# Performance work log

Measured on AMD Instinct MI355X. Metric: run time of the kernel, lower is better.

## Reference

```python
import jax, jax.numpy as jnp
import numpy as np

B, L, C_IN, D, H, DFF, NL, NC, PH = 32, 512, 16, 512, 8, 2048, 3, 10, 128
DH = D // H


def circ_conv1d(x, w):
    # x: [B, C, S] with circular padding 1 on spatial dim, w: [O, C, 3]
    xp = jnp.concatenate([x[..., -1:], x, x[..., :1]], axis=-1)
    return jax.lax.conv_general_dilated(xp, w, (1,), 'VALID',
                                        dimension_numbers=('NCH', 'OIH', 'NCH'))


def positional_embedding(length, d):
    pos = jnp.arange(length, dtype=jnp.float32)[:, None]
    div = jnp.exp(jnp.arange(0, d, 2, dtype=jnp.float32) * (-np.log(10000.0) / d))
    pe = jnp.zeros((length, d), jnp.float32)
    pe = pe.at[:, 0::2].set(jnp.sin(pos * div))
    pe = pe.at[:, 1::2].set(jnp.cos(pos * div))
    return pe


def layer_norm(x, g, b):
    m = jnp.mean(x, -1, keepdims=True)
    v = jnp.var(x, -1, keepdims=True)
    return (x - m) / jnp.sqrt(v + 1e-5) * g + b


def projector(x, stats, conv_w, w0, b0, w1, b1, w2):
    # x: [B, L, C_IN] (channels = seq_len, spatial = enc_in), stats: [B, 1, C_IN]
    y = circ_conv1d(x, conv_w)                     # [B, 1, C_IN]
    y = jnp.concatenate([y, stats], axis=1)        # [B, 2, C_IN]
    y = y.reshape(x.shape[0], -1)                  # [B, 2*C_IN]
    h = jax.nn.relu(y @ w0.T + b0)
    h = jax.nn.relu(h @ w1.T + b1)
    return h @ w2.T                                # no bias on output


def setup_inputs() -> dict:
    key = jax.random.key(0)
    ks = iter(jax.random.split(key, 64))
    rn = lambda shape, s=0.02: jax.random.normal(next(ks), shape, jnp.float32) * s
    inp = {
        'x_enc': jax.random.normal(next(ks), (B, L, C_IN), jnp.float32),
        'x_mark_enc': jnp.ones((B, L), jnp.float32),
        'tok_w': rn((D, C_IN, 3)),
        'Wq': rn((NL, D, D)), 'bq': jnp.zeros((NL, D)),
        'Wk': rn((NL, D, D)), 'bk': jnp.zeros((NL, D)),
        'Wv': rn((NL, D, D)), 'bv': jnp.zeros((NL, D)),
        'Wo': rn((NL, D, D)), 'bo': jnp.zeros((NL, D)),
        'W1': rn((NL, DFF, D)), 'b1': jnp.zeros((NL, DFF)),
        'W2': rn((NL, D, DFF)), 'b2': jnp.zeros((NL, D)),
        'ln1_g': jnp.ones((NL, D)), 'ln1_b': jnp.zeros((NL, D)),
        'ln2_g': jnp.ones((NL, D)), 'ln2_b': jnp.zeros((NL, D)),
        'norm_g': jnp.ones((D,)), 'norm_b': jnp.zeros((D,)),
        'proj_w': rn((NC, D * L)), 'proj_b': jnp.zeros((NC,)),
        'tau_conv_w': rn((1, L, 3)), 'tau_w0': rn((PH, 2 * C_IN)), 'tau_b0': jnp.zeros((PH,)),
        'tau_w1': rn((PH, PH)), 'tau_b1': jnp.zeros((PH,)), 'tau_w2': rn((1, PH)),
        'del_conv_w': rn((1, L, 3)), 'del_w0': rn((PH, 2 * C_IN)), 'del_b0': jnp.zeros((PH,)),
        'del_w1': rn((PH, PH)), 'del_b1': jnp.zeros((PH,)), 'del_w2': rn((L, PH)),
    }
    return inp


def reference(x_enc, x_mark_enc, tok_w,
              Wq, bq, Wk, bk, Wv, bv, Wo, bo,
              W1, b1, W2, b2, ln1_g, ln1_b, ln2_g, ln2_b,
              norm_g, norm_b, proj_w, proj_b,
              tau_conv_w, tau_w0, tau_b0, tau_w1, tau_b1, tau_w2,
              del_conv_w, del_w0, del_b0, del_w1, del_b1, del_w2):
    # De-stationary statistics (detached in the original)
    x_raw = jax.lax.stop_gradient(x_enc)
    mean_enc = jnp.mean(x_raw, 1, keepdims=True)                 # [B,1,C]
    std_enc = jnp.sqrt(jnp.var(x_raw, 1, keepdims=True) + 1e-5)  # [B,1,C]
    tau = jnp.exp(projector(x_raw, std_enc, tau_conv_w, tau_w0, tau_b0,
                            tau_w1, tau_b1, tau_w2))             # [B,1]
    delta = projector(x_raw, mean_enc, del_conv_w, del_w0, del_b0,
                      del_w1, del_b1, del_w2)                    # [B,L]

    # DataEmbedding: circular token conv + sinusoidal positional encoding
    tok = circ_conv1d(jnp.transpose(x_enc, (0, 2, 1)), tok_w)    # [B,D,L]
    x = jnp.transpose(tok, (0, 2, 1)) + positional_embedding(L, D)[None]

    scale = 1.0 / np.sqrt(DH)
    tau4 = tau.reshape(B, 1, 1, 1)
    delta4 = delta[:, None, None, :]
    for i in range(NL):
        q = (x @ Wq[i].T + bq[i]).reshape(B, L, H, DH)
        k = (x @ Wk[i].T + bk[i]).reshape(B, L, H, DH)
        v = (x @ Wv[i].T + bv[i]).reshape(B, L, H, DH)
        scores = jnp.einsum('blhe,bshe->bhls', q, k) * tau4 + delta4
        A = jax.nn.softmax(scale * scores, axis=-1)
        o = jnp.einsum('bhls,bshd->blhd', A, v).reshape(B, L, D)
        o = o @ Wo[i].T + bo[i]
        x = layer_norm(x + o, ln1_g[i], ln1_b[i])
        y = jax.nn.gelu(x @ W1[i].T + b1[i], approximate=False) @ W2[i].T + b2[i]
        x = layer_norm(x + y, ln2_g[i], ln2_b[i])
    x = layer_norm(x, norm_g, norm_b)

    out = jax.nn.gelu(x, approximate=False)
    out = out * x_mark_enc[..., None]
    out = out.reshape(B, -1) @ proj_w.T + proj_b                 # [B, NC]
    return out
```

## Files before the change

### kernel.cpp

```cpp
#include <hip/hip_runtime.h>
#include <hip/hip_bf16.h>
#include <cstdint>

#define DEVINL __device__ __forceinline__

typedef unsigned short u16;
typedef short bf16x8 __attribute__((ext_vector_type(8)));
typedef float f32x4 __attribute__((ext_vector_type(4)));
typedef float f32x16 __attribute__((ext_vector_type(16)));

DEVINL u16 f2b(float f) {
    union { float f; uint32_t u; } x{f};
    uint32_t r = x.u + 0x7fffu + ((x.u >> 16) & 1u);
    return (u16)(r >> 16);
}
DEVINL float b2f(u16 h) {
    union { uint32_t u; float f; } x{(uint32_t)h << 16};
    return x.f;
}
DEVINL float gelu_exact(float v) {
    return 0.5f * v * (1.0f + erff(v * 0.70710678118654752f));
}
DEVINL void gload_lds16(const void* g, void* l) {
    __builtin_amdgcn_global_load_lds(
        (const __attribute__((address_space(1))) void*)(uintptr_t)g,
        (__attribute__((address_space(3))) void*)(uint32_t)(uintptr_t)l,
        16, 0, 0);
}
DEVINL void cvt8(const float* src, u16* dst) {
    float4 a = *(const float4*)src;
    float4 b = *(const float4*)(src + 4);
    u16 t[8] = {f2b(a.x), f2b(a.y), f2b(a.z), f2b(a.w),
                f2b(b.x), f2b(b.y), f2b(b.z), f2b(b.w)};
    *(uint4*)dst = *(const uint4*)t;
}

__global__ __launch_bounds__(256)
void cvtqkv_kernel(const float* __restrict__ Wq, const float* __restrict__ Wk,
                   const float* __restrict__ Wv, u16* __restrict__ dst) {
    size_t i = ((size_t)blockIdx.x * 256 + threadIdx.x) * 8;
    int slice = (int)(i >> 18);
    int layer = slice / 3, which = slice - layer * 3;
    size_t rem = i & 262143;
    const float* src = (which == 0 ? Wq : which == 1 ? Wk : Wv) + (size_t)layer * 262144 + rem;
    u16* d = dst + (size_t)layer * 786432 + (size_t)which * 262144 + rem;
    cvt8(src, d);
}
__global__ __launch_bounds__(256)
void cvt4_kernel(const float* __restrict__ s0, const float* __restrict__ s1,
                 const float* __restrict__ s2, const float* __restrict__ s3,
                 u16* __restrict__ d0, u16* __restrict__ d1,
                 u16* __restrict__ d2, u16* __restrict__ d3) {
    size_t i = ((size_t)blockIdx.x * 256 + threadIdx.x) * 8;
    if (i < 786432) { cvt8(s0 + i, d0 + i); return; }
    i -= 786432;
    if (i < 3145728) { cvt8(s1 + i, d1 + i); return; }
    i -= 3145728;
    if (i < 3145728) { cvt8(s2 + i, d2 + i); return; }
    i -= 3145728;
    if (i < 2621440) { cvt8(s3 + i, d3 + i); }
}

__global__ void packb_kernel(const float* __restrict__ bq, const float* __restrict__ bk,
                             const float* __restrict__ bv, float* __restrict__ out) {
    int idx = blockIdx.x * 256 + threadIdx.x;
    if (idx >= 3 * 1536) return;
    int i = idx / 1536, j = idx - i * 1536;
    float v = (j < 512) ? bq[i * 512 + j]
            : (j < 1024) ? bk[i * 512 + j - 512]
                         : bv[i * 512 + j - 1024];
    out[idx] = v;
}

__global__ void pe_kernel(float* __restrict__ pet) {
    int l = blockIdx.x, d2 = threadIdx.x;
    float freq = expf(-(float)(2 * d2) * 0.0179889460390f);
    float ang = (float)l * freq;
    pet[l * 512 + 2 * d2]     = sinf(ang);
    pet[l * 512 + 2 * d2 + 1] = cosf(ang);
}

__global__ void stats_kernel(const float* __restrict__ xe, float* __restrict__ mean,
                             float* __restrict__ stdv) {
    int b = blockIdx.x, ln = threadIdx.x;
    int c = ln & 15, part = ln >> 4;
    float s = 0.f, sq = 0.f;
    for (int l = part; l < 512; l += 4) {
        float x = xe[(size_t)b * 8192 + l * 16 + c];
        s += x; sq += x * x;
    }
    s += __shfl_xor(s, 16);  s += __shfl_xor(s, 32);
    sq += __shfl_xor(sq, 16); sq += __shfl_xor(sq, 32);
    if (part == 0) {
        float m = s * (1.0f / 512.0f);
        mean[b * 16 + c] = m;
        stdv[b * 16 + c] = sqrtf(sq * (1.0f / 512.0f) - m * m + 1e-5f);
    }
}

__global__ __launch_bounds__(128)
void proj_kernel(const float* __restrict__ xe, const float* __restrict__ stats,
                 const float* __restrict__ cw, const float* __restrict__ w0,
                 const float* __restrict__ b0, const float* __restrict__ w1,
                 const float* __restrict__ b1, const float* __restrict__ w2,
                 float* __restrict__ outp, int outn, int do_exp) {
    __shared__ float zl[32], h0l[128], h1l[128], red[2];
    int b = blockIdx.x, tid = threadIdx.x;
    {
        int c = tid >> 3, part = tid & 7;
        float acc = 0.f;
        for (int l = part; l < 512; l += 8) {
            const float* xr = xe + (size_t)b * 8192 + l * 16;
            float w0v = cw[l * 3 + 0], w1v = cw[l * 3 + 1], w2v = cw[l * 3 + 2];
            acc += xr[(c + 15) & 15] * w0v + xr[c] * w1v + xr[(c + 1) & 15] * w2v;
        }
        acc += __shfl_xor(acc, 1); acc += __shfl_xor(acc, 2); acc += __shfl_xor(acc, 4);
        if (part == 0) zl[c] = acc;
        if (tid < 16) zl[16 + tid] = stats[b * 16 + tid];
    }
    __syncthreads();
    {
        float acc = b0[tid];
        #pragma unroll
        for (int i = 0; i < 32; ++i) acc += zl[i] * w0[tid * 32 + i];
        h0l[tid] = fmaxf(acc, 0.0f);
    }
    __syncthreads();
    {
        float acc = b1[tid];
        for (int i = 0; i < 128; ++i) acc += h0l[i] * w1[tid * 128 + i];
        h1l[tid] = fmaxf(acc, 0.0f);
    }
    __syncthreads();
    if (outn == 1) {
        float p = h1l[tid] * w2[tid];
        p += __shfl_xor(p, 1);  p += __shfl_xor(p, 2);  p += __shfl_xor(p, 4);
        p += __shfl_xor(p, 8);  p += __shfl_xor(p, 16); p += __shfl_xor(p, 32);
        if ((tid & 63) == 0) red[tid >> 6] = p;
        __syncthreads();
        if (tid == 0) {
            float v = red[0] + red[1];
            outp[b] = do_exp ? expf(v) : v;
        }
    } else {
        for (int l = tid; l < outn; l += 128) {
            float acc = 0.f;
            for (int i = 0; i < 128; ++i) acc += h1l[i] * w2[l * 128 + i];
            outp[(size_t)b * outn + l] = acc;
        }
    }
}

__global__ __launch_bounds__(256)
void tokconv_kernel(const float* __restrict__ xe, const float* __restrict__ tw,
                    const float* __restrict__ pet,
                    float* __restrict__ xf, u16* __restrict__ xb) {
    __shared__ float xs[34][16];
    int lt = blockIdx.x, b = blockIdx.y, tid = threadIdx.x;
    int l0 = lt * 32;
    for (int idx = tid; idx < 34 * 16; idx += 256) {
        int r = idx >> 4, c = idx & 15;
        int gl = (l0 - 1 + r + 512) & 511;
        xs[r][c] = xe[(size_t)b * 8192 + gl * 16 + c];
    }
    __syncthreads();
    for (int dd = tid; dd < 512; dd += 256) {
        float twr[48];
        #pragma unroll
        for (int i = 0; i < 48; ++i) twr[i] = tw[dd * 48 + i];
        for (int l = 0; l < 32; ++l) {
            float acc = 0.f;
            #pragma unroll
            for (int c = 0; c < 16; ++c) {
                acc += xs[l][c]     * twr[c * 3 + 0];
                acc += xs[l + 1][c] * twr[c * 3 + 1];
                acc += xs[l + 2][c] * twr[c * 3 + 2];
            }
            float vv = acc + pet[(size_t)(l0 + l) * 512 + dd];
            size_t idx = ((size_t)b * 512 + l0 + l) * 512 + dd;
            xf[idx] = vv;
            xb[idx] = f2b(vv);
        }
    }
}

template <int ACT>
__global__ __launch_bounds__(256)
void gemm32(const u16* __restrict__ A, const u16* __restrict__ B,
            const float* __restrict__ bias, u16* __restrict__ Cv0,
            u16* __restrict__ Cv1, int M, int N, int K, int Kc) {
    __shared__ u16 smem[3][2][128 * 32];
    const int tid = threadIdx.x, wv = tid >> 6, ln = tid & 63;
    const int nwg = gridDim.x * gridDim.y;
    const int bid = blockIdx.y * gridDim.x + blockIdx.x;
    const int wg  = (bid & 7) * (nwg >> 3) + (bid >> 3);
    const int n0 = (wg % gridDim.x) * 128;
    const int m0 = (wg / gridDim.x) * 128;
    const int kz = blockIdx.z;
    const int wm = (wv >> 1) * 64, wn = (wv & 1) * 64;
    const int l31 = ln & 31, h2 = ln >> 5;
    f32x16 acc[2][2] = {};
    const int r0s = wv * 16 + (ln >> 2);
    const int sl = ln & 3;
    const int k0 = kz * Kc;

    auto stage = [&](int buf, int kt) {
        #pragma unroll
        for (int c = 0; c < 2; ++c) {
            int row = r0s + c * 64;
            int ssl = sl ^ ((row >> 1) & 3);
            int ldsoff = row * 32 + sl * 8;
            gload_lds16(A + (size_t)(m0 + row) * K + kt + ssl * 8, (char*)smem[buf][0] + ldsoff * 2);
            gload_lds16(B + (size_t)(n0 + row) * K + kt + ssl * 8, (char*)smem[buf][1] + ldsoff * 2);
        }
    };

    const int nt = Kc >> 5;
    stage(0, k0);
    if (nt > 1) stage(1, k0 + 32);
    for (int t = 0; t < nt; ++t) {
        if (t + 1 < nt) { asm volatile("s_waitcnt vmcnt(4)"); }
        else            { asm volatile("s_waitcnt vmcnt(0)"); }
        __builtin_amdgcn_s_barrier();
        if (t + 2 < nt) stage((t + 2) % 3, k0 + (t + 2) * 32);
        const u16* As = smem[t % 3][0];
        const u16* Bs = smem[t % 3][1];
        bf16x8 af[2][2], bfr[2][2];
        #pragma unroll
        for (int mi = 0; mi < 2; ++mi) {
            int row = wm + mi * 32 + l31;
            int swz = (row >> 1) & 3;
            #pragma unroll
            for (int kk = 0; kk < 2; ++kk) {
                int phys = (kk * 2 + h2) ^ swz;
                af[mi][kk] = *(const bf16x8*)(As + row * 32 + phys * 8);
            }
        }
        #pragma unroll
        for (int nj = 0; nj < 2; ++nj) {
            int row = wn + nj * 32 + l31;
            int swz = (row >> 1) & 3;
            #pragma unroll
            for (int kk = 0; kk < 2; ++kk) {
                int phys = (kk * 2 + h2) ^ swz;
                bfr[nj][kk] = *(const bf16x8*)(Bs + row * 32 + phys * 8);
            }
        }
        #pragma unroll
        for (int mi = 0; mi < 2; ++mi)
            #pragma unroll
            for (int nj = 0; nj < 2; ++nj)
                #pragma unroll
                for (int kk = 0; kk < 2; ++kk)
                    acc[mi][nj] = __builtin_amdgcn_mfma_f32_32x32x16_bf16(
                        af[mi][kk], bfr[nj][kk], acc[mi][nj], 0, 0, 0);
    }
    __syncthreads();

    const bool second = (kz != 0);
    float* eps = (float*)smem + wv * (16 * 68);
    u16* Cout = second ? Cv1 : Cv0;
    #pragma unroll
    for (int ch = 0; ch < 4; ++ch) {
        const int mi = ch >> 1, rsel = ch & 1;
        #pragma unroll
        for (int nj = 0; nj < 2; ++nj) {
            int col = nj * 32 + l31;
            float bv = second ? 0.0f : bias[n0 + wn + col];
            #pragma unroll
            for (int r1l = 0; r1l < 2; ++r1l)
                #pragma unroll
                for (int rr = 0; rr < 4; ++rr) {
                    int reg = rr + 4 * (rsel * 2 + r1l);
                    int rloc = h2 * 4 + rr + 8 * r1l;
                    float v = acc[mi][nj][reg] + bv;
                    if (ACT == 1 && !second) v = gelu_exact(v);
                    eps[rloc * 68 + col] = v;
                }
        }
        #pragma unroll
        for (int pp = 0; pp < 4; ++pp) {
            int rl = pp * 4 + (ln >> 4);
            float4 vv = *(const float4*)(eps + rl * 68 + (ln & 15) * 4);
            size_t row = (size_t)(m0 + wm + ch * 16 + rl);
            int col = n0 + wn + (ln & 15) * 4;
            u16 t4[4] = {f2b(vv.x), f2b(vv.y), f2b(vv.z), f2b(vv.w)};
            *(uint2*)(Cout + row * N + col) = *(const uint2*)t4;
        }
    }
}

__global__ __launch_bounds__(512)
void attn2_kernel(const u16* __restrict__ qkv, const float* __restrict__ tau,
                  const float* __restrict__ delta, u16* __restrict__ o) {
    __shared__ u16 KL[64 * 64];
    __shared__ u16 VT[64 * 72];
    __shared__ u16 PL[8][32 * 64];
    const int tid = threadIdx.x, w = tid >> 6, ln = tid & 63;
    const int lo = ln & 15, hi = ln >> 4;
    const int qh = blockIdx.x, h = blockIdx.y, b = blockIdx.z;
    const size_t qrow0 = (size_t)b * 512;
    const u16* qp = qkv;
    const u16* kp = qkv + 512;
    const u16* vp = qkv + 1024;
    const int hofs = h * 64;
    const float ts = tau[b] * 0.125f;
    u16* Pw = (u16*)PL[w];
    const int q0 = qh * 256 + w * 32;

    bf16x8 qa[2][2];
    #pragma unroll
    for (int i = 0; i < 2; ++i)
        #pragma unroll
        for (int ks = 0; ks < 2; ++ks)
            qa[i][ks] = *(const bf16x8*)(qp + (qrow0 + q0 + i * 16 + lo) * 1536 + hofs + ks * 32 + hi * 8);

    float m_run[2] = {-1e30f, -1e30f};
    float l_run[2] = {0.f, 0.f};
    f32x4 oacc[2][4] = {};

    const int vsl = tid & 7, vsr = tid >> 3;
    uint4 vreg = *(const uint4*)(vp + (qrow0 + vsr) * 1536 + hofs + vsl * 8);

    for (int nt = 0; nt < 8; ++nt) {
        __syncthreads();
        {
            int s = tid >> 3, j = tid & 7;
            int jl = j ^ (s & 7);
            gload_lds16(kp + (qrow0 + nt * 64 + s) * 1536 + hofs + jl * 8,
                        (char*)KL + tid * 16);
        }
        {
            u16 tmp[8]; *(uint4*)tmp = vreg;
            #pragma unroll
            for (int e = 0; e < 8; ++e) {
                int d = vsl * 8 + e;
                int byt = d * 144 + (((vsr >> 3) ^ vsl) << 4) + (vsr & 7) * 2;
                *(u16*)((char*)VT + byt) = tmp[e];
            }
        }
        if (nt < 7)
            vreg = *(const uint4*)(vp + (qrow0 + (nt + 1) * 64 + vsr) * 1536 + hofs + vsl * 8);
        __syncthreads();

        f32x4 sacc[2][4] = {};
        #pragma unroll
        for (int ks = 0; ks < 2; ++ks) {
            #pragma unroll
            for (int jn = 0; jn < 4; ++jn) {
                int s = jn * 16 + lo;
                int phys = (ks * 4 + hi) ^ (s & 7);
                bf16x8 kb = *(const bf16x8*)((const char*)KL + s * 128 + phys * 16);
                #pragma unroll
                for (int i = 0; i < 2; ++i)
                    sacc[i][jn] = __builtin_amdgcn_mfma_f32_16x16x32_bf16(kb, qa[i][ks], sacc[i][jn], 0, 0, 0);
            }
        }
        float tmax[2] = {-1e30f, -1e30f};
        #pragma unroll
        for (int jn = 0; jn < 4; ++jn) {
            float4 dv4 = *(const float4*)(delta + b * 512 + nt * 64 + jn * 16 + hi * 4);
            float dv[4] = {dv4.x, dv4.y, dv4.z, dv4.w};
            #pragma unroll
            for (int i = 0; i < 2; ++i)
                #pragma unroll
                for (int r = 0; r < 4; ++r) {
                    float v = sacc[i][jn][r] * ts + dv[r] * 0.125f;
                    sacc[i][jn][r] = v;
                    tmax[i] = fmaxf(tmax[i], v);
                }
        }
        #pragma unroll
        for (int i = 0; i < 2; ++i) {
            tmax[i] = fmaxf(tmax[i], __shfl_xor(tmax[i], 16));
            tmax[i] = fmaxf(tmax[i], __shfl_xor(tmax[i], 32));
            float mnew = fmaxf(m_run[i], tmax[i]);
            float fac = __expf(m_run[i] - mnew);
            m_run[i] = mnew;
            l_run[i] *= fac;
            #pragma unroll
            for (int jd = 0; jd < 4; ++jd)
                #pragma unroll
                for (int r = 0; r < 4; ++r) oacc[i][jd][r] *= fac;
        }
        #pragma unroll
        for (int i = 0; i < 2; ++i) {
            float ls = 0.f;
            #pragma unroll
            for (int jn = 0; jn < 4; ++jn) {
                float p0 = __expf(sacc[i][jn][0] - m_run[i]);
                float p1 = __expf(sacc[i][jn][1] - m_run[i]);
                float p2 = __expf(sacc[i][jn][2] - m_run[i]);
                float p3 = __expf(sacc[i][jn][3] - m_run[i]);
                ls += (p0 + p1) + (p2 + p3);
                uint2 pk;
                pk.x = (uint32_t)f2b(p0) | ((uint32_t)f2b(p1) << 16);
                pk.y = (uint32_t)f2b(p2) | ((uint32_t)f2b(p3) << 16);
                int q = i * 16 + lo;
                int ls16 = jn * 2 + (hi >> 1);
                int byt = q * 128 + (((ls16 ^ (q & 7)) << 4)) + (hi & 1) * 8;
                *(uint2*)((char*)Pw + byt) = pk;
            }
            ls += __shfl_xor(ls, 16);
            ls += __shfl_xor(ls, 32);
            l_run[i] += ls;
        }
        #pragma unroll
        for (int ks2 = 0; ks2 < 2; ++ks2) {
            bf16x8 pa[2];
            #pragma unroll
            for (int i = 0; i < 2; ++i) {
                int q = i * 16 + lo;
                int phys = (ks2 * 4 + hi) ^ (q & 7);
                pa[i] = *(const bf16x8*)((const char*)Pw + q * 128 + phys * 16);
            }
            #pragma unroll
            for (int jd = 0; jd < 4; ++jd) {
                int d = jd * 16 + lo;
                int cs = (ks2 * 4 + hi) ^ ((d >> 3) & 7);
                bf16x8 vb = *(const bf16x8*)((const char*)VT + d * 144 + cs * 16);
                #pragma unroll
                for (int i = 0; i < 2; ++i)
                    oacc[i][jd] = __builtin_amdgcn_mfma_f32_16x16x32_bf16(vb, pa[i], oacc[i][jd], 0, 0, 0);
            }
        }
    }
    #pragma unroll
    for (int i = 0; i < 2; ++i) {
        float inv = 1.0f / l_run[i];
        #pragma unroll
        for (int jd = 0; jd < 4; ++jd) {
            u16 t4[4];
            #pragma unroll
            for (int r = 0; r < 4; ++r) t4[r] = f2b(oacc[i][jd][r] * inv);
            size_t row = qrow0 + q0 + i * 16 + lo;
            *(uint2*)(o + row * 512 + hofs + jd * 16 + hi * 4) = *(const uint2*)t4;
        }
    }
}

__global__ __launch_bounds__(256)
void ln3_kernel(const float* __restrict__ xin, const u16* res0,
                const u16* res1, const float* __restrict__ g,
                const float* __restrict__ bta,
                float* __restrict__ xout, u16* xbf) {
    const int row = blockIdx.x * 4 + (threadIdx.x >> 6);
    const int ln = threadIdx.x & 63;
    const float* xr = xin + (size_t)row * 512;
    const u16* r0p = res0 + (size_t)row * 512;
    const u16* r1p = res1 + (size_t)row * 512;
    float4 a = *(const float4*)(xr + ln * 4);
    float4 c = *(const float4*)(xr + 256 + ln * 4);
    uint2 qa_ = *(const uint2*)(r0p + ln * 4);
    uint2 qc_ = *(const uint2*)(r0p + 256 + ln * 4);
    uint2 pa_ = *(const uint2*)(r1p + ln * 4);
    uint2 pc_ = *(const uint2*)(r1p + 256 + ln * 4);
    const u16* qa16 = (const u16*)&qa_;  const u16* qc16 = (const u16*)&qc_;
    const u16* pa16 = (const u16*)&pa_;  const u16* pc16 = (const u16*)&pc_;
    a.x += b2f(qa16[0]) + b2f(pa16[0]); a.y += b2f(qa16[1]) + b2f(pa16[1]);
    a.z += b2f(qa16[2]) + b2f(pa16[2]); a.w += b2f(qa16[3]) + b2f(pa16[3]);
    c.x += b2f(qc16[0]) + b2f(pc16[0]); c.y += b2f(qc16[1]) + b2f(pc16[1]);
    c.z += b2f(qc16[2]) + b2f(pc16[2]); c.w += b2f(qc16[3]) + b2f(pc16[3]);
    float s = a.x + a.y + a.z + a.w + c.x + c.y + c.z + c.w;
    float sq = a.x*a.x + a.y*a.y + a.z*a.z + a.w*a.w + c.x*c.x + c.y*c.y + c.z*c.z + c.w*c.w;
    #pragma unroll
    for (int m = 1; m < 64; m <<= 1) { s += __shfl_xor(s, m); sq += __shfl_xor(sq, m); }
    float mean = s * 0.001953125f;
    float var = sq * 0.001953125f - mean * mean;
    float rstd = rsqrtf(var + 1e-5f);
    float4 g0 = *(const float4*)(g + ln * 4);
    float4 g1 = *(const float4*)(g + 256 + ln * 4);
    float4 b0 = *(const float4*)(bta + ln * 4);
    float4 b1 = *(const float4*)(bta + 256 + ln * 4);
    float4 o0, o1;
    o0.x = (a.x - mean) * rstd * g0.x + b0.x;
    o0.y = (a.y - mean) * rstd * g0.y + b0.y;
    o0.z = (a.z - mean) * rstd * g0.z + b0.z;
    o0.w = (a.w - mean) * rstd * g0.w + b0.w;
    o1.x = (c.x - mean) * rstd * g1.x + b1.x;
    o1.y = (c.y - mean) * rstd * g1.y + b1.y;
    o1.z = (c.z - mean) * rstd * g1.z + b1.z;
    o1.w = (c.w - mean) * rstd * g1.w + b1.w;
    *(float4*)(xout + (size_t)row * 512 + ln * 4) = o0;
    *(float4*)(xout + (size_t)row * 512 + 256 + ln * 4) = o1;
    u16 t0[4] = {f2b(o0.x), f2b(o0.y), f2b(o0.z), f2b(o0.w)};
    u16 t1[4] = {f2b(o1.x), f2b(o1.y), f2b(o1.z), f2b(o1.w)};
    *(uint2*)(xbf + (size_t)row * 512 + ln * 4) = *(const uint2*)t0;
    *(uint2*)(xbf + (size_t)row * 512 + 256 + ln * 4) = *(const uint2*)t1;
}

__global__ __launch_bounds__(256)
void lngelu_kernel(const float* __restrict__ xin, const float* __restrict__ g,
                   const float* __restrict__ bta, const float* __restrict__ mark,
                   u16* __restrict__ outb) {
    const int row = blockIdx.x * 4 + (threadIdx.x >> 6);
    const int ln = threadIdx.x & 63;
    const float* xr = xin + (size_t)row * 512;
    float4 a = *(const float4*)(xr + ln * 4);
    float4 c = *(const float4*)(xr + 256 + ln * 4);
    float s = a.x + a.y + a.z + a.w + c.x + c.y + c.z + c.w;
    float sq = a.x*a.x + a.y*a.y + a.z*a.z + a.w*a.w + c.x*c.x + c.y*c.y + c.z*c.z + c.w*c.w;
    #pragma unroll
    for (int m = 1; m < 64; m <<= 1) { s += __shfl_xor(s, m); sq += __shfl_xor(sq, m); }
    float mean = s * 0.001953125f;
    float var = sq * 0.001953125f - mean * mean;
    float rstd = rsqrtf(var + 1e-5f);
    float mk = mark[row];
    float4 g0 = *(const float4*)(g + ln * 4);
    float4 g1 = *(const float4*)(g + 256 + ln * 4);
    float4 b0 = *(const float4*)(bta + ln * 4);
    float4 b1 = *(const float4*)(bta + 256 + ln * 4);
    float v0 = gelu_exact((a.x - mean) * rstd * g0.x + b0.x) * mk;
    float v1 = gelu_exact((a.y - mean) * rstd * g0.y + b0.y) * mk;
    float v2 = gelu_exact((a.z - mean) * rstd * g0.z + b0.z) * mk;
    float v3 = gelu_exact((a.w - mean) * rstd * g0.w + b0.w) * mk;
    float v4 = gelu_exact((c.x - mean) * rstd * g1.x + b1.x) * mk;
    float v5 = gelu_exact((c.y - mean) * rstd * g1.y + b1.y) * mk;
    float v6 = gelu_exact((c.z - mean) * rstd * g1.z + b1.z) * mk;
    float v7 = gelu_exact((c.w - mean) * rstd * g1.w + b1.w) * mk;
    u16 t0[4] = {f2b(v0), f2b(v1), f2b(v2), f2b(v3)};
    u16 t1[4] = {f2b(v4), f2b(v5), f2b(v6), f2b(v7)};
    *(uint2*)(outb + (size_t)row * 512 + ln * 4) = *(const uint2*)t0;
    *(uint2*)(outb + (size_t)row * 512 + 256 + ln * 4) = *(const uint2*)t1;
}

__global__ __launch_bounds__(256)
void fproj_kernel(const u16* __restrict__ gb, const u16* __restrict__ pw,
                  const float* __restrict__ pb, float* __restrict__ out) {
    __shared__ float red[32][4];
    int n = blockIdx.x, ks = blockIdx.y, tid = threadIdx.x;
    float acc[32];
    #pragma unroll
    for (int m = 0; m < 32; ++m) acc[m] = 0.f;
    for (int j = 0; j < 8; ++j) {
        size_t k0 = (size_t)ks * 16384 + j * 2048 + tid * 8;
        bf16x8 w8 = *(const bf16x8*)(pw + (size_t)n * 262144 + k0);
        float wf[8];
        #pragma unroll
        for (int e = 0; e < 8; ++e) wf[e] = b2f((u16)w8[e]);
        #pragma unroll
        for (int m = 0; m < 32; ++m) {
            bf16x8 g8 = *(const bf16x8*)(gb + (size_t)m * 262144 + k0);
            float a = acc[m];
            #pragma unroll
            for (int e = 0; e < 8; ++e) a += b2f((u16)g8[e]) * wf[e];
            acc[m] = a;
        }
    }
    int w = tid >> 6;
    #pragma unroll
    for (int m = 0; m < 32; ++m) {
        float s = acc[m];
        s += __shfl_xor(s, 1);  s += __shfl_xor(s, 2);  s += __shfl_xor(s, 4);
        s += __shfl_xor(s, 8);  s += __shfl_xor(s, 16); s += __shfl_xor(s, 32);
        if ((tid & 63) == 0) red[m][w] = s;
    }
    __syncthreads();
    if (tid < 32) {
        int m = tid;
        float s = red[m][0] + red[m][1] + red[m][2] + red[m][3];
        if (ks == 0) s += pb[n];
        atomicAdd(&out[m * 10 + n], s);
    }
}

extern "C" void kernel_launch(void* const* d_in, const int* in_sizes, int n_in,
                              void* d_out, int out_size, void* d_ws, size_t ws_size,
                              hipStream_t stream) {
    const float* x_enc  = (const float*)d_in[0];
    const float* x_mark = (const float*)d_in[1];
    const float* tok_w  = (const float*)d_in[2];
    const float* Wq = (const float*)d_in[3];   const float* bq = (const float*)d_in[4];
    const float* Wk = (const float*)d_in[5];   const float* bk = (const float*)d_in[6];
    const float* Wv = (const float*)d_in[7];   const float* bv = (const float*)d_in[8];
    const float* Wo = (const float*)d_in[9];   const float* bo = (const float*)d_in[10];
    const float* W1 = (const float*)d_in[11];  const float* b1 = (const float*)d_in[12];
    const float* W2 = (const float*)d_in[13];  const float* b2 = (const float*)d_in[14];
    const float* ln1_g = (const float*)d_in[15]; const float* ln1_b = (const float*)d_in[16];
    const float* ln2_g = (const float*)d_in[17]; const float* ln2_b = (const float*)d_in[18];
    const float* norm_g = (const float*)d_in[19]; const float* norm_b = (const float*)d_in[20];
    const float* proj_w = (const float*)d_in[21]; const float* proj_b = (const float*)d_in[22];
    const float* tau_cw = (const float*)d_in[23];
    const float* tau_w0 = (const float*)d_in[24]; const float* tau_b0 = (const float*)d_in[25];
    const float* tau_w1 = (const float*)d_in[26]; const float* tau_b1 = (const float*)d_in[27];
    const float* tau_w2 = (const float*)d_in[28];
    const float* del_cw = (const float*)d_in[29];
    const float* del_w0 = (const float*)d_in[30]; const float* del_b0 = (const float*)d_in[31];
    const float* del_w1 = (const float*)d_in[32]; const float* del_b1 = (const float*)d_in[33];
    const float* del_w2 = (const float*)d_in[34];
    float* out = (float*)d_out;

    char* ws = (char*)d_ws;
    size_t off = 0;
    auto alloc = [&](size_t bytes) -> void* {
        void* p = ws + off;
        off += (bytes + 255) & ~(size_t)255;
        return p;
    };
    u16* wqkvb = (u16*)alloc((size_t)3 * 786432 * 2);
    u16* wob = (u16*)alloc(786432 * 2);
    u16* w1b = (u16*)alloc(3145728 * 2);
    u16* w2b = (u16*)alloc(3145728 * 2);
    u16* pwb = (u16*)alloc(2621440 * 2);
    float* bqkvb = (float*)alloc(3 * 1536 * 4);
    float* petab = (float*)alloc((size_t)262144 * 4);
    float* meanb = (float*)alloc(512 * 4);
    float* stdb  = (float*)alloc(512 * 4);
    float* taub  = (float*)alloc(32 * 4);
    float* delb  = (float*)alloc(16384 * 4);
    float* xf = (float*)alloc((size_t)8388608 * 4);
    u16*  xb  = (u16*)alloc((size_t)8388608 * 2);
    u16*  sfb = (u16*)alloc((size_t)8388608 * 2);
    u16* qkvb = (u16*)alloc((size_t)16384 * 1536 * 2);
    u16* ob   = (u16*)alloc((size_t)8388608 * 2);
    u16* hb   = qkvb;
    u16* gbuf = qkvb;
    u16* p1o  = qkvb;
    u16* p1f  = xb;

    cvtqkv_kernel<<<dim3(1152), dim3(256), 0, stream>>>(Wq, Wk, Wv, wqkvb);
    cvt4_kernel<<<dim3(5030), dim3(256), 0, stream>>>(Wo, W1, W2, proj_w, wob, w1b, w2b, pwb);
    packb_kernel<<<dim3(18), dim3(256), 0, stream>>>(bq, bk, bv, bqkvb);
    pe_kernel<<<dim3(512), dim3(256), 0, stream>>>(petab);

    stats_kernel<<<dim3(32), dim3(64), 0, stream>>>(x_enc, meanb, stdb);
    proj_kernel<<<dim3(32), dim3(128), 0, stream>>>(x_enc, stdb, tau_cw, tau_w0, tau_b0,
                                                    tau_w1, tau_b1, tau_w2, taub, 1, 1);
    proj_kernel<<<dim3(32), dim3(128), 0, stream>>>(x_enc, meanb, del_cw, del_w0, del_b0,
                                                    del_w1, del_b1, del_w2, delb, 512, 0);
    tokconv_kernel<<<dim3(16, 32), dim3(256), 0, stream>>>(x_enc, tok_w, petab, xf, xb);

    for (int i = 0; i < 3; ++i) {
        const u16* wqkv_i = wqkvb + (size_t)i * 786432;
        const u16* wo_i = wob + (size_t)i * 262144;
        const u16* w1_i = w1b + (size_t)i * 1048576;
        const u16* w2_i = w2b + (size_t)i * 1048576;
        gemm32<0><<<dim3(12, 128, 1), dim3(256), 0, stream>>>(
            xb, wqkv_i, bqkvb + i * 1536, qkvb, nullptr, 16384, 1536, 512, 512);
        attn2_kernel<<<dim3(2, 8, 32), dim3(512), 0, stream>>>(qkvb, taub, delb, ob);
        gemm32<0><<<dim3(4, 128, 2), dim3(256), 0, stream>>>(
            ob, wo_i, bo + i * 512, sfb, p1o, 16384, 512, 512, 256);
        ln3_kernel<<<dim3(4096), dim3(256), 0, stream>>>(xf, sfb, p1o,
            ln1_g + i * 512, ln1_b + i * 512, xf, xb);
        gemm32<1><<<dim3(16, 128, 1), dim3(256), 0, stream>>>(
            xb, w1_i, b1 + i * 2048, hb, nullptr, 16384, 2048, 512, 512);
        gemm32<0><<<dim3(4, 128, 2), dim3(256), 0, stream>>>(
            hb, w2_i, b2 + i * 512, sfb, p1f, 16384, 512, 2048, 1024);
        ln3_kernel<<<dim3(4096), dim3(256), 0, stream>>>(xf, sfb, p1f,
            ln2_g + i * 512, ln2_b + i * 512, xf, xb);
    }

    lngelu_kernel<<<dim3(4096), dim3(256), 0, stream>>>(xf, norm_g, norm_b, x_mark, gbuf);
    hipMemsetAsync(d_out, 0, (size_t)out_size * 4, stream);
    fproj_kernel<<<dim3(10, 16), dim3(256), 0, stream>>>(gbuf, pwb, proj_b, out);
}
```

Baseline: 980.8 us.

## Fuse output and FFN-down GEMMs with residual add and LayerNorm

Adds a gemmln kernel in which each 512-thread block computes a full 64x512 row tile and applies bias, the residual add and LayerNorm in its epilogue. It replaces both the split-K gemm32 launches and the separate ln3 kernel, removing the bf16 partial-sum buffers and their round trip. The cost is a grid of only 256 blocks. B fragments are also read straight from global memory without LDS staging, which may hurt GEMM efficiency, especially for K=2048.

```diff
diff --git a/kernel.cpp b/kernel.cpp
--- a/kernel.cpp
+++ b/kernel.cpp
@@ -188,7 +188,7 @@
 __global__ __launch_bounds__(256)
 void gemm32(const u16* __restrict__ A, const u16* __restrict__ B,
             const float* __restrict__ bias, u16* __restrict__ Cv0,
-            u16* __restrict__ Cv1, int M, int N, int K, int Kc) {
+            int M, int N, int K) {
     __shared__ u16 smem[3][2][128 * 32];
     const int tid = threadIdx.x, wv = tid >> 6, ln = tid & 63;
     const int nwg = gridDim.x * gridDim.y;
@@ -196,13 +196,11 @@
     const int wg  = (bid & 7) * (nwg >> 3) + (bid >> 3);
     const int n0 = (wg % gridDim.x) * 128;
     const int m0 = (wg / gridDim.x) * 128;
-    const int kz = blockIdx.z;
     const int wm = (wv >> 1) * 64, wn = (wv & 1) * 64;
     const int l31 = ln & 31, h2 = ln >> 5;
     f32x16 acc[2][2] = {};
     const int r0s = wv * 16 + (ln >> 2);
     const int sl = ln & 3;
-    const int k0 = kz * Kc;
 
     auto stage = [&](int buf, int kt) {
         #pragma unroll
@@ -215,14 +213,14 @@
         }
     };
 
-    const int nt = Kc >> 5;
-    stage(0, k0);
-    if (nt > 1) stage(1, k0 + 32);
+    const int nt = K >> 5;
+    stage(0, 0);
+    if (nt > 1) stage(1, 32);
     for (int t = 0; t < nt; ++t) {
         if (t + 1 < nt) { asm volatile("s_waitcnt vmcnt(4)"); }
         else            { asm volatile("s_waitcnt vmcnt(0)"); }
         __builtin_amdgcn_s_barrier();
-        if (t + 2 < nt) stage((t + 2) % 3, k0 + (t + 2) * 32);
+        if (t + 2 < nt) stage((t + 2) % 3, (t + 2) * 32);
         const u16* As = smem[t % 3][0];
         const u16* Bs = smem[t % 3][1];
         bf16x8 af[2][2], bfr[2][2];
@@ -257,16 +255,14 @@
     }
     __syncthreads();
 
-    const bool second = (kz != 0);
     float* eps = (float*)smem + wv * (16 * 68);
-    u16* Cout = second ? Cv1 : Cv0;
     #pragma unroll
     for (int ch = 0; ch < 4; ++ch) {
         const int mi = ch >> 1, rsel = ch & 1;
         #pragma unroll
         for (int nj = 0; nj < 2; ++nj) {
             int col = nj * 32 + l31;
-            float bv = second ? 0.0f : bias[n0 + wn + col];
+            float bv = bias[n0 + wn + col];
             #pragma unroll
             for (int r1l = 0; r1l < 2; ++r1l)
                 #pragma unroll
@@ -274,7 +270,7 @@
                     int reg = rr + 4 * (rsel * 2 + r1l);
                     int rloc = h2 * 4 + rr + 8 * r1l;
                     float v = acc[mi][nj][reg] + bv;
-                    if (ACT == 1 && !second) v = gelu_exact(v);
+                    if (ACT == 1) v = gelu_exact(v);
                     eps[rloc * 68 + col] = v;
                 }
         }
@@ -285,9 +281,120 @@
             size_t row = (size_t)(m0 + wm + ch * 16 + rl);
             int col = n0 + wn + (ln & 15) * 4;
             u16 t4[4] = {f2b(vv.x), f2b(vv.y), f2b(vv.z), f2b(vv.w)};
-            *(uint2*)(Cout + row * N + col) = *(const uint2*)t4;
-        }
-    }
+            *(uint2*)(Cv0 + row * N + col) = *(const uint2*)t4;
+        }
+    }
+}
+
+__global__ __launch_bounds__(512)
+void gemmln_kernel(const u16* __restrict__ A, const u16* __restrict__ B,
+                   const float* __restrict__ bias, const float* __restrict__ g,
+                   const float* __restrict__ bta,
+                   float* xf, u16* __restrict__ xb, int K) {
+    __shared__ u16 As[2][64 * 64];
+    __shared__ float redS[4][64], redQ[4][64], mst[64], rst[64];
+    const int tid = threadIdx.x, wv = tid >> 6, ln = tid & 63;
+    const int wm = wv >> 2, wn = wv & 3;
+    const int lo = ln & 15, hi = ln >> 4;
+    const int m0 = blockIdx.x * 64;
+    f32x4 acc[2][8] = {};
+
+    const int srow = tid >> 3, sj = tid & 7;
+    const int sjl = sj ^ (srow & 7);
+    auto stage = [&](int buf, int kt) {
+        gload_lds16(A + (size_t)(m0 + srow) * K + kt + sjl * 8,
+                    (char*)As[buf] + tid * 16);
+    };
+
+    const int nt = K >> 6;
+    int cur = 0;
+    stage(0, 0);
+    __syncthreads();
+    for (int t = 0; t < nt; ++t) {
+        if (t + 1 < nt) stage(cur ^ 1, (t + 1) * 64);
+        const int kt = t * 64;
+        bf16x8 bfr[8][2];
+        #pragma unroll
+        for (int j = 0; j < 8; ++j) {
+            int n = wn * 128 + j * 16 + lo;
+            #pragma unroll
+            for (int kk = 0; kk < 2; ++kk)
+                bfr[j][kk] = *(const bf16x8*)(B + (size_t)n * K + kt + kk * 32 + hi * 8);
+        }
+        bf16x8 af[2][2];
+        #pragma unroll
+        for (int i = 0; i < 2; ++i) {
+            int r = wm * 32 + i * 16 + lo;
+            #pragma unroll
+            for (int kk = 0; kk < 2; ++kk) {
+                int phys = (kk * 4 + hi) ^ (r & 7);
+                af[i][kk] = *(const bf16x8*)((const char*)As[cur] + r * 128 + phys * 16);
+            }
+        }
+        #pragma unroll
+        for (int i = 0; i < 2; ++i)
+            #pragma unroll
+            for (int j = 0; j < 8; ++j)
+                #pragma unroll
+                for (int kk = 0; kk < 2; ++kk)
+                    acc[i][j] = __builtin_amdgcn_mfma_f32_16x16x32_bf16(
+                        af[i][kk], bfr[j][kk], acc[i][j], 0, 0, 0);
+        __syncthreads();
+        cur ^= 1;
+    }
+
+    float bv[8], gl[8], bl[8];
+    #pragma unroll
+    for (int j = 0; j < 8; ++j) {
+        int col = wn * 128 + j * 16 + lo;
+        bv[j] = bias[col]; gl[j] = g[col]; bl[j] = bta[col];
+    }
+    #pragma unroll
+    for (int i = 0; i < 2; ++i)
+        #pragma unroll
+        for (int rr = 0; rr < 4; ++rr) {
+            int row = wm * 32 + i * 16 + hi * 4 + rr;
+            const float* xr = xf + (size_t)(m0 + row) * 512;
+            float ps = 0.f, pq = 0.f;
+            #pragma unroll
+            for (int j = 0; j < 8; ++j) {
+                int col = wn * 128 + j * 16 + lo;
+                float v = acc[i][j][rr] + bv[j] + xr[col];
+                acc[i][j][rr] = v;
+                ps += v; pq += v * v;
+            }
+            ps += __shfl_xor(ps, 1); pq += __shfl_xor(pq, 1);
+            ps += __shfl_xor(ps, 2); pq += __shfl_xor(pq, 2);
+            ps += __shfl_xor(ps, 4); pq += __shfl_xor(pq, 4);
+            ps += __shfl_xor(ps, 8); pq += __shfl_xor(pq, 8);
+            if (lo == 0) { redS[wn][row] = ps; redQ[wn][row] = pq; }
+        }
+    __syncthreads();
+    if (tid < 64) {
+        float s = redS[0][tid] + redS[1][tid] + redS[2][tid] + redS[3][tid];
+        float q = redQ[0][tid] + redQ[1][tid] + redQ[2][tid] + redQ[3][tid];
+        float mean = s * (1.0f / 512.0f);
+        float var = q * (1.0f / 512.0f) - mean * mean;
+        mst[tid] = mean;
+        rst[tid] = rsqrtf(var + 1e-5f);
+    }
+    __syncthreads();
+    #pragma unroll
+    for (int i = 0; i < 2; ++i)
+        #pragma unroll
+        for (int rr = 0; rr < 4; ++rr) {
+            int row = wm * 32 + i * 16 + hi * 4 + rr;
+            float mean = mst[row], rstd = rst[row];
+            float* xfo = xf + (size_t)(m0 + row) * 512;
+            u16* xbo = xb + (size_t)(m0 + row) * 512;
+            #pragma unroll
+            for (int j = 0; j < 8; ++j) {
+                int col = wn * 128 + j * 16 + lo;
+                float nv = (acc[i][j][rr] - mean) * rstd * gl[j] + bl[j];
+                xfo[col] = nv;
+                xbo[col] = f2b(nv);
+            }
+        }
 }
 
 __global__ __launch_bounds__(512)
@@ -437,56 +544,6 @@
             *(uint2*)(o + row * 512 + hofs + jd * 16 + hi * 4) = *(const uint2*)t4;
         }
     }
-}
-
-__global__ __launch_bounds__(256)
-void ln3_kernel(const float* __restrict__ xin, const u16* res0,
-                const u16* res1, const float* __restrict__ g,
-                const float* __restrict__ bta,
-                float* __restrict__ xout, u16* xbf) {
-    const int row = blockIdx.x * 4 + (threadIdx.x >> 6);
-    const int ln = threadIdx.x & 63;
-    const float* xr = xin + (size_t)row * 512;
-    const u16* r0p = res0 + (size_t)row * 512;
-    const u16* r1p = res1 + (size_t)row * 512;
-    float4 a = *(const float4*)(xr + ln * 4);
-    float4 c = *(const float4*)(xr + 256 + ln * 4);
-    uint2 qa_ = *(const uint2*)(r0p + ln * 4);
-    uint2 qc_ = *(const uint2*)(r0p + 256 + ln * 4);
-    uint2 pa_ = *(const uint2*)(r1p + ln * 4);
-    uint2 pc_ = *(const uint2*)(r1p + 256 + ln * 4);
-    const u16* qa16 = (const u16*)&qa_;  const u16* qc16 = (const u16*)&qc_;
-    const u16* pa16 = (const u16*)&pa_;  const u16* pc16 = (const u16*)&pc_;
-    a.x += b2f(qa16[0]) + b2f(pa16[0]); a.y += b2f(qa16[1]) + b2f(pa16[1]);
-    a.z += b2f(qa16[2]) + b2f(pa16[2]); a.w += b2f(qa16[3]) + b2f(pa16[3]);
-    c.x += b2f(qc16[0]) + b2f(pc16[0]); c.y += b2f(qc16[1]) + b2f(pc16[1]);
-    c.z += b2f(qc16[2]) + b2f(pc16[2]); c.w += b2f(qc16[3]) + b2f(pc16[3]);
-    float s = a.x + a.y + a.z + a.w + c.x + c.y + c.z + c.w;
-    float sq = a.x*a.x + a.y*a.y + a.z*a.z + a.w*a.w + c.x*c.x + c.y*c.y + c.z*c.z + c.w*c.w;
-    #pragma unroll
-    for (int m = 1; m < 64; m <<= 1) { s += __shfl_xor(s, m); sq += __shfl_xor(sq, m); }
-    float mean = s * 0.001953125f;
-    float var = sq * 0.001953125f - mean * mean;
-    float rstd = rsqrtf(var + 1e-5f);
-    float4 g0 = *(const float4*)(g + ln * 4);
-    float4 g1 = *(const float4*)(g + 256 + ln * 4);
-    float4 b0 = *(const float4*)(bta + ln * 4);
-    float4 b1 = *(const float4*)(bta + 256 + ln * 4);
-    float4 o0, o1;
-    o0.x = (a.x - mean) * rstd * g0.x + b0.x;
-    o0.y = (a.y - mean) * rstd * g0.y + b0.y;
-    o0.z = (a.z - mean) * rstd * g0.z + b0.z;
-    o0.w = (a.w - mean) * rstd * g0.w + b0.w;
-    o1.x = (c.x - mean) * rstd * g1.x + b1.x;
-    o1.y = (c.y - mean) * rstd * g1.y + b1.y;
-    o1.z = (c.z - mean) * rstd * g1.z + b1.z;
-    o1.w = (c.w - mean) * rstd * g1.w + b1.w;
-    *(float4*)(xout + (size_t)row * 512 + ln * 4) = o0;
-    *(float4*)(xout + (size_t)row * 512 + 256 + ln * 4) = o1;
-    u16 t0[4] = {f2b(o0.x), f2b(o0.y), f2b(o0.z), f2b(o0.w)};
-    u16 t1[4] = {f2b(o1.x), f2b(o1.y), f2b(o1.z), f2b(o1.w)};
-    *(uint2*)(xbf + (size_t)row * 512 + ln * 4) = *(const uint2*)t0;
-    *(uint2*)(xbf + (size_t)row * 512 + 256 + ln * 4) = *(const uint2*)t1;
 }
 
 __global__ __launch_bounds__(256)
@@ -610,13 +667,10 @@
     float* delb  = (float*)alloc(16384 * 4);
     float* xf = (float*)alloc((size_t)8388608 * 4);
     u16*  xb  = (u16*)alloc((size_t)8388608 * 2);
-    u16*  sfb = (u16*)alloc((size_t)8388608 * 2);
     u16* qkvb = (u16*)alloc((size_t)16384 * 1536 * 2);
     u16* ob   = (u16*)alloc((size_t)8388608 * 2);
     u16* hb   = qkvb;
     u16* gbuf = qkvb;
-    u16* p1o  = qkvb;
-    u16* p1f  = xb;
 
     cvtqkv_kernel<<<dim3(1152), dim3(256), 0, stream>>>(Wq, Wk, Wv, wqkvb);
     cvt4_kernel<<<dim3(5030), dim3(256), 0, stream>>>(Wo, W1, W2, proj_w, wob, w1b, w2b, pwb);
@@ -635,19 +689,15 @@
         const u16* wo_i = wob + (size_t)i * 262144;
         const u16* w1_i = w1b + (size_t)i * 1048576;
         const u16* w2_i = w2b + (size_t)i * 1048576;
-        gemm32<0><<<dim3(12, 128, 1), dim3(256), 0, stream>>>(
-            xb, wqkv_i, bqkvb + i * 1536, qkvb, nullptr, 16384, 1536, 512, 512);
+        gemm32<0><<<dim3(12, 128), dim3(256), 0, stream>>>(
+            xb, wqkv_i, bqkvb + i * 1536, qkvb, 16384, 1536, 512);
         attn2_kernel<<<dim3(2, 8, 32), dim3(512), 0, stream>>>(qkvb, taub, delb, ob);
-        gemm32<0><<<dim3(4, 128, 2), dim3(256), 0, stream>>>(
-            ob, wo_i, bo + i * 512, sfb, p1o, 16384, 512, 512, 256);
-        ln3_kernel<<<dim3(4096), dim3(256), 0, stream>>>(xf, sfb, p1o,
-            ln1_g + i * 512, ln1_b + i * 512, xf, xb);
-        gemm32<1><<<dim3(16, 128, 1), dim3(256), 0, stream>>>(
-            xb, w1_i, b1 + i * 2048, hb, nullptr, 16384, 2048, 512, 512);
-        gemm32<0><<<dim3(4, 128, 2), dim3(256), 0, stream>>>(
-            hb, w2_i, b2 + i * 512, sfb, p1f, 16384, 512, 2048, 1024);
-        ln3_kernel<<<dim3(4096), dim3(256), 0, stream>>>(xf, sfb, p1f,
-            ln2_g + i * 512, ln2_b + i * 512, xf, xb);
+        gemmln_kernel<<<dim3(256), dim3(512), 0, stream>>>(
+            ob, wo_i, bo + i * 512, ln1_g + i * 512, ln1_b + i * 512, xf, xb, 512);
+        gemm32<1><<<dim3(16, 128), dim3(256), 0, stream>>>(
+            xb, w1_i, b1 + i * 2048, hb, 16384, 2048, 512);
+        gemmln_kernel<<<dim3(256), dim3(512), 0, stream>>>(
+            hb, w2_i, b2 + i * 512, ln2_g + i * 512, ln2_b + i * 512, xf, xb, 2048);
     }
 
     lngelu_kernel<<<dim3(4096), dim3(256), 0, stream>>>(xf, norm_g, norm_b, x_mark, gbuf);
```

Measured after the change: 1.226 ms. +25.0%, slower.
